# Performance work log

Measured on AMD Instinct MI355X. Metric: run time of the kernel, lower is better.

Reference implementation:

```python
import jax, jax.numpy as jnp
import numpy as np

N_LAYERS, B, H, D = 24, 16, 32, 64
E = H * D            # 2048
TS_H = 32            # token_shift_hidden_dim
N_BRANCH = 5         # key, receptance, decay, value, bonus
GN_EPS = 1e-3        # keras GroupNormalization default epsilon


def setup_inputs() -> dict:
    key = jax.random.key(0)
    ks = jax.random.split(key, 20)
    s = 0.02
    return {
        "inputs": jax.random.normal(ks[0], (B, E), jnp.float32),
        "state": jax.random.normal(ks[1], (N_LAYERS, 1, B, E), jnp.float32),
        "state_matrix": jax.random.normal(ks[2], (N_LAYERS, B, H, D, D), jnp.float32),
        # stacked branch params, order: key, receptance, decay, value, bonus
        "mus": jax.random.normal(ks[3], (N_BRANCH, E), jnp.float32) * s,
        "lambdas": jax.random.normal(ks[4], (N_BRANCH, E), jnp.float32) * s,
        "Aw": jax.random.normal(ks[5], (N_BRANCH, E, TS_H), jnp.float32) * s,
        "Ab": jnp.zeros((N_BRANCH, TS_H), jnp.float32),
        "Bw": jax.random.normal(ks[6], (N_BRANCH, TS_H, E), jnp.float32) * s,
        "Bb": jnp.zeros((N_BRANCH, E), jnp.float32),
        "MW": jax.random.normal(ks[7], (N_BRANCH, H, D, D), jnp.float32) * s,
        "Mb": jnp.zeros((N_BRANCH, H, D), jnp.float32),
        "gate_mu": jax.random.normal(ks[8], (E,), jnp.float32) * s,
        "gate_W": jax.random.normal(ks[9], (E, E), jnp.float32) * s,
        "gate_b": jnp.zeros((E,), jnp.float32),
        "gn_gamma": jnp.ones((E,), jnp.float32),
        "gn_beta": jnp.zeros((E,), jnp.float32),
        "out_W": jax.random.normal(ks[10], (E, E), jnp.float32) * s,
        "out_b": jnp.zeros((E,), jnp.float32),
        "layer_id": 12,
    }


def reference(inputs, state, state_matrix, mus, lambdas, Aw, Ab, Bw, Bb, MW, Mb,
              gate_mu, gate_W, gate_b, gn_gamma, gn_beta, out_W, out_b, layer_id):
    x = inputs                       # [B, E]
    last_x = state[layer_id, 0]      # [B, E]
    diff = x - last_x

    # ddlerp token shift for all 5 branches at once:
    # lora(x + diff*mu) = lambda + tanh(. @ A) @ B ; out = x + lora * diff
    lora_in = x[None] + diff[None] * mus[:, None]                      # [5, B, E]
    hdn = jnp.tanh(jnp.einsum('sbe,seh->sbh', lora_in, Aw) + Ab[:, None])
    lora = jnp.einsum('sbh,she->sbe', hdn, Bw) + Bb[:, None] + lambdas[:, None]
    ts = (lora * diff[None] + x[None]).reshape(N_BRANCH, B, H, D)      # [5, B, H, D]

    # per-head dense for each branch
    proj = jnp.einsum('sbhd,shde->sbhe', ts, MW) + Mb[:, None]         # [5, B, H, D]
    k, r, w_raw, v, u = proj[0], proj[1], proj[2], proj[3], proj[4]

    g = (x * gate_mu + last_x * (1.0 - gate_mu)) @ gate_W + gate_b     # [B, E]

    kv = k[..., :, None] * v[..., None, :]                             # [B, H, D, D]
    w = jnp.exp(-jnp.exp(w_raw))[..., None]                            # [B, H, D, 1]
    S = state_matrix[layer_id]                                         # [B, H, D, D]
    wkv = kv * u[..., None] + S
    new_S = w * S + kv
    rwkv = jnp.einsum('bhij,bhj->bhi', wkv, r)                         # [B, H, D]

    # group norm: num_heads groups over channel axis
    mean = rwkv.mean(-1, keepdims=True)
    var = rwkv.var(-1, keepdims=True)
    normed = ((rwkv - mean) / jnp.sqrt(var + GN_EPS)).reshape(B, E)
    normed = normed * gn_gamma + gn_beta

    time_mixed = (normed * jax.nn.silu(g)) @ out_W + out_b             # [B, E]

    new_state = state.at[layer_id, 0].set(inputs)
    new_state_matrix = state_matrix.at[layer_id].set(new_S)
    return time_mixed, new_state, new_state_matrix
```

## Files before the change

kernel.cpp:

```cpp
#include <hip/hip_runtime.h>
#include <math.h>

#define NL 24
#define BB 16
#define HH 32
#define DD 64
#define EE 2048
#define TSH 32
#define NB 5
#define BE (BB*EE)
#define STATE_N (NL*BB*EE)
#define SM_N (NL*BB*HH*DD*DD)
#define GN_EPS 1e-3f

__global__ __launch_bounds__(256) void k_head(
    const float4* __restrict__ state4, const float4* __restrict__ inputs4,
    float4* __restrict__ out_state4,
    float* __restrict__ out_tm, float* __restrict__ g,
    const float* __restrict__ out_b, const float* __restrict__ gate_b,
    const float* __restrict__ inputs, const float* __restrict__ state,
    const float* __restrict__ mus, const float* __restrict__ Aw,
    const float* __restrict__ Ab, const float* __restrict__ lambdas,
    const float* __restrict__ Bw, const float* __restrict__ Bb,
    const float* __restrict__ MW, const float* __restrict__ Mb,
    const float* __restrict__ gate_mu, float* __restrict__ proj,
    float* __restrict__ gx, const int* __restrict__ lid_p)
{
    int blk = blockIdx.x, tid = threadIdx.x;
    int lid = *lid_p;
    if (blk < 768) {
        int i = blk * 256 + tid;
        int lo = lid * (BE / 4);
        float4 v = (i >= lo && i < lo + BE / 4) ? inputs4[i - lo] : state4[i];
        out_state4[i] = v;
        return;
    }
    if (blk < 1024) {
        int idx = (blk - 768) * 256 + tid;
        if (idx < BE) out_tm[idx] = out_b[idx & (EE - 1)];
        else g[idx - BE] = gate_b[(idx - BE) & (EE - 1)];
        return;
    }
    int sb = blk - 1024;
    int s = sb / BB, b = sb % BB;
    __shared__ float xs[EE], dsh[EE], lis[EE], tsl[EE];
    __shared__ float red[TSH][9];
    __shared__ float hdnl[TSH];
    const float* x  = inputs + b * EE;
    const float* lx = state + lid * BE + b * EE;
    const float* mu = mus + s * EE;
    for (int e = tid; e < EE; e += 256) {
        float xv = x[e], lxv = lx[e];
        float d = xv - lxv;
        xs[e] = xv; dsh[e] = d;
        lis[e] = xv + d * mu[e];
        if (s == 0) {
            float gm = gate_mu[e];
            gx[b * EE + e] = xv * gm + lxv * (1.f - gm);
        }
    }
    __syncthreads();
    {
        int h = tid & 31, part = tid >> 5;
        const float* A = Aw + s * EE * TSH;
        float acc = 0.f;
        int e0 = part * 256;
        #pragma unroll 8
        for (int e = e0; e < e0 + 256; ++e) acc += lis[e] * A[e * TSH + h];
        red[h][part] = acc;
    }
    __syncthreads();
    if (tid < TSH) {
        float sum = Ab[s * TSH + tid];
        #pragma unroll
        for (int p = 0; p < 8; ++p) sum += red[tid][p];
        hdnl[tid] = tanhf(sum);
    }
    __syncthreads();
    for (int e = tid; e < EE; e += 256) {
        const float* Bp = Bw + s * TSH * EE + e;
        float acc = Bb[s * EE + e] + lambdas[s * EE + e];
        #pragma unroll
        for (int h2 = 0; h2 < TSH; ++h2) acc += hdnl[h2] * Bp[h2 * EE];
        tsl[e] = acc * dsh[e] + xs[e];
    }
    __syncthreads();
    for (int o = tid; o < EE; o += 256) {
        int h2 = o >> 6, e = o & 63;
        const float* M = MW + (s * HH + h2) * DD * DD;
        const float* t = tsl + h2 * DD;
        float acc = Mb[(s * HH + h2) * DD + e];
        #pragma unroll 8
        for (int d = 0; d < DD; ++d) acc += t[d] * M[d * DD + e];
        proj[(s * BB + b) * EE + o] = acc;
    }
}

template <bool SILU>
__device__ __forceinline__ void mm_block(
    int blk, const float* __restrict__ Arows, const float* __restrict__ Grows,
    const float* __restrict__ W, float* __restrict__ out)
{
    int tid = threadIdx.x;
    int et = blk & 7, kc = blk >> 3;
    int e = et * 256 + tid;
    int k0 = kc * 64;
    __shared__ float As[BB][64];
    for (int i = tid; i < BB * 64; i += 256) {
        int b = i >> 6, kk = i & 63;
        float av = Arows[b * EE + k0 + kk];
        if constexpr (SILU) {
            float gv = Grows[b * EE + k0 + kk];
            av *= gv / (1.f + expf(-gv));
        }
        As[b][kk] = av;
    }
    __syncthreads();
    float acc[BB];
    #pragma unroll
    for (int b = 0; b < BB; ++b) acc[b] = 0.f;
    #pragma unroll 8
    for (int kk = 0; kk < 64; ++kk) {
        float wv = W[(k0 + kk) * EE + e];
        #pragma unroll
        for (int b = 0; b < BB; ++b) acc[b] += As[b][kk] * wv;
    }
    #pragma unroll
    for (int b = 0; b < BB; ++b) atomicAdd(&out[b * EE + e], acc[b]);
}

__global__ __launch_bounds__(256) void k_mid(
    const float* __restrict__ gx, const float* __restrict__ gate_W,
    float* __restrict__ g,
    const float4* __restrict__ sm4, float4* __restrict__ out_sm4,
    const float* __restrict__ proj,
    const float* __restrict__ gn_gamma, const float* __restrict__ gn_beta,
    float* __restrict__ a_out, const int* __restrict__ lid_p)
{
    int blk = blockIdx.x, tid = threadIdx.x;
    if (blk < 256) { mm_block<false>(blk, gx, nullptr, gate_W, g); return; }
    int lid = *lid_p;
    int r = blk - 256;
    int b = r / HH, h = r % HH;
    int base4 = (lid * BB * HH + r) * (DD * DD / 4);
    int j = tid & 63, q = tid >> 6;
    const float* P = proj + (b * HH + h) * DD + j;
    float kv   = P[0 * BE];
    float rv   = P[1 * BE];
    float wraw = P[2 * BE];
    float vv   = P[3 * BE];
    float uv   = P[4 * BE];
    float wv = expf(-expf(wraw));
    float vr = vv * rv;
    #pragma unroll
    for (int o = 32; o; o >>= 1) vr += __shfl_xor(vr, o);
    __shared__ float rw[DD];
    const float* S = (const float*)(sm4 + base4);
    float* NS = (float*)(out_sm4 + base4);
    for (int ii = 0; ii < 16; ii += 4) {
        int i0 = q * 16 + ii;
        float sv[4], kk[4], ww[4], uu[4], pp[4];
        #pragma unroll
        for (int t = 0; t < 4; ++t) {
            sv[t] = S[(i0 + t) * DD + j];
            kk[t] = __shfl(kv, i0 + t);
            ww[t] = __shfl(wv, i0 + t);
            uu[t] = __shfl(uv, i0 + t);
        }
        #pragma unroll
        for (int t = 0; t < 4; ++t) {
            NS[(i0 + t) * DD + j] = ww[t] * sv[t] + kk[t] * vv;
            pp[t] = sv[t] * rv;
        }
        #pragma unroll
        for (int o = 32; o; o >>= 1) {
            #pragma unroll
            for (int t = 0; t < 4; ++t) pp[t] += __shfl_xor(pp[t], o);
        }
        if (j == 0) {
            #pragma unroll
            for (int t = 0; t < 4; ++t) rw[i0 + t] = kk[t] * uu[t] * vr + pp[t];
        }
    }
    __syncthreads();
    if (tid < DD) {
        float xv = rw[tid];
        float m = xv;
        #pragma unroll
        for (int o = 32; o; o >>= 1) m += __shfl_xor(m, o);
        m *= (1.f / 64.f);
        float d = xv - m;
        float var = d * d;
        #pragma unroll
        for (int o = 32; o; o >>= 1) var += __shfl_xor(var, o);
        var *= (1.f / 64.f);
        float normed = d * rsqrtf(var + GN_EPS);
        int e = h * DD + tid;
        a_out[b * EE + e] = normed * gn_gamma[e] + gn_beta[e];
    }
}

__global__ __launch_bounds__(256) void k_tail(
    const float* __restrict__ a, const float* __restrict__ g,
    const float* __restrict__ out_W, float* __restrict__ out_tm,
    const float4* __restrict__ sm4, float4* __restrict__ out_sm4,
    const int* __restrict__ lid_p)
{
    int blk = blockIdx.x, tid = threadIdx.x;
    if (blk < 256) { mm_block<true>(blk, a, g, out_W, out_tm); return; }
    int lid = *lid_p;
    int c = blk - 256;
    int l = c >> 9;
    int rr = c & 511;
    int ls = l + (l >= lid);
    const float4* src = sm4 + ((long)ls * 512 + rr) * 1024;
    float4* dst = out_sm4 + ((long)ls * 512 + rr) * 1024;
    #pragma unroll
    for (int p = 0; p < 4; ++p) dst[p * 256 + tid] = src[p * 256 + tid];
}

extern "C" void kernel_launch(void* const* d_in, const int* in_sizes, int n_in,
                              void* d_out, int out_size, void* d_ws, size_t ws_size,
                              hipStream_t stream) {
    const float* inputs   = (const float*)d_in[0];
    const float* state    = (const float*)d_in[1];
    const float* sm       = (const float*)d_in[2];
    const float* mus      = (const float*)d_in[3];
    const float* lambdas  = (const float*)d_in[4];
    const float* Aw       = (const float*)d_in[5];
    const float* Ab       = (const float*)d_in[6];
    const float* Bw       = (const float*)d_in[7];
    const float* Bb       = (const float*)d_in[8];
    const float* MW       = (const float*)d_in[9];
    const float* Mb       = (const float*)d_in[10];
    const float* gate_mu  = (const float*)d_in[11];
    const float* gate_W   = (const float*)d_in[12];
    const float* gate_b   = (const float*)d_in[13];
    const float* gn_gamma = (const float*)d_in[14];
    const float* gn_beta  = (const float*)d_in[15];
    const float* out_W    = (const float*)d_in[16];
    const float* out_b    = (const float*)d_in[17];
    const int*   lid      = (const int*)d_in[18];

    float* out_tm    = (float*)d_out;
    float* out_state = out_tm + BE;
    float* out_sm    = out_state + STATE_N;

    float* ws   = (float*)d_ws;
    float* proj = ws;
    float* gx   = proj + NB * BE;
    float* g    = gx + BE;
    float* a    = g + BE;

    k_head<<<1104, 256, 0, stream>>>((const float4*)state, (const float4*)inputs,
                                     (float4*)out_state, out_tm, g, out_b, gate_b,
                                     inputs, state, mus, Aw, Ab, lambdas, Bw, Bb,
                                     MW, Mb, gate_mu, proj, gx, lid);
    k_mid<<<768, 256, 0, stream>>>(gx, gate_W, g, (const float4*)sm, (float4*)out_sm,
                                   proj, gn_gamma, gn_beta, a, lid);
    k_tail<<<12032, 256, 0, stream>>>(a, g, out_W, out_tm,
                                      (const float4*)sm, (float4*)out_sm, lid);
}
```

Before: 470.5 us.

## Split head into three kernels and spread state-matrix copy across all launches

The monolithic head kernel, which ran 80 serial-heavy blocks, is split into three stages: hidden tanh, token-shift LoRA expansion and per-head projection. Each stage now uses many more parallel blocks. The bulk copy of the unchanged state-matrix layers is cut into chunks and attached to every one of the six launches, so the bandwidth-bound copy runs alongside the latency-bound compute stages instead of all at the end. The cost is more kernel launches and intermediate round-trips through workspace memory.

```diff
diff --git a/kernel.cpp b/kernel.cpp
--- a/kernel.cpp
+++ b/kernel.cpp
@@ -10,99 +10,148 @@
 #define NB 5
 #define BE (BB*EE)
 #define STATE_N (NL*BB*EE)
-#define SM_N (NL*BB*HH*DD*DD)
 #define GN_EPS 1e-3f
 
-__global__ __launch_bounds__(256) void k_head(
-    const float4* __restrict__ state4, const float4* __restrict__ inputs4,
-    float4* __restrict__ out_state4,
-    float* __restrict__ out_tm, float* __restrict__ g,
-    const float* __restrict__ out_b, const float* __restrict__ gate_b,
+#define NCH 11776
+#define C1 2400
+#define C2 2200
+#define C3 2400
+#define C4 2200
+#define C5 1776
+#define C6 800
+
+__device__ __forceinline__ void sm_chunk(int c, int lid, const float4* __restrict__ sm4,
+                                         float4* __restrict__ out4, int tid) {
+    int l = c >> 9, rr = c & 511;
+    int ls = l + (l >= lid);
+    const float4* src = sm4 + (long)(ls * 512 + rr) * 1024;
+    float4*       dst = out4 + (long)(ls * 512 + rr) * 1024;
+    #pragma unroll
+    for (int p = 0; p < 4; ++p) dst[p * 256 + tid] = src[p * 256 + tid];
+}
+
+__global__ __launch_bounds__(256) void k1_hdn(
     const float* __restrict__ inputs, const float* __restrict__ state,
     const float* __restrict__ mus, const float* __restrict__ Aw,
-    const float* __restrict__ Ab, const float* __restrict__ lambdas,
-    const float* __restrict__ Bw, const float* __restrict__ Bb,
-    const float* __restrict__ MW, const float* __restrict__ Mb,
-    const float* __restrict__ gate_mu, float* __restrict__ proj,
-    float* __restrict__ gx, const int* __restrict__ lid_p)
-{
-    int blk = blockIdx.x, tid = threadIdx.x;
-    int lid = *lid_p;
-    if (blk < 768) {
-        int i = blk * 256 + tid;
+    const float* __restrict__ Ab, float* __restrict__ hdn,
+    const float4* __restrict__ state4, const float4* __restrict__ inputs4,
+    float4* __restrict__ out_state4, float* __restrict__ out_tm,
+    float* __restrict__ g, const float* __restrict__ out_b,
+    const float* __restrict__ gate_b,
+    const float4* __restrict__ sm4, float4* __restrict__ out_sm4,
+    const int* __restrict__ lid_p)
+{
+    int blk = blockIdx.x, tid = threadIdx.x;
+    int lid = *lid_p;
+    if (blk >= 1104) {
+        sm_chunk(blk - 1104, lid, sm4, out_sm4, tid);
+        return;
+    }
+    if (blk >= 848) {
+        int idx = (blk - 848) * 256 + tid;
+        if (idx < BE) out_tm[idx] = out_b[idx & (EE - 1)];
+        else g[idx - BE] = gate_b[(idx - BE) & (EE - 1)];
+        return;
+    }
+    if (blk >= 80) {
+        int i = (blk - 80) * 256 + tid;
         int lo = lid * (BE / 4);
         float4 v = (i >= lo && i < lo + BE / 4) ? inputs4[i - lo] : state4[i];
         out_state4[i] = v;
         return;
     }
-    if (blk < 1024) {
-        int idx = (blk - 768) * 256 + tid;
-        if (idx < BE) out_tm[idx] = out_b[idx & (EE - 1)];
-        else g[idx - BE] = gate_b[(idx - BE) & (EE - 1)];
-        return;
-    }
-    int sb = blk - 1024;
-    int s = sb / BB, b = sb % BB;
-    __shared__ float xs[EE], dsh[EE], lis[EE], tsl[EE];
-    __shared__ float red[TSH][9];
-    __shared__ float hdnl[TSH];
+    int s = blk / BB, b = blk % BB;
+    __shared__ float li[EE];
     const float* x  = inputs + b * EE;
     const float* lx = state + lid * BE + b * EE;
     const float* mu = mus + s * EE;
     for (int e = tid; e < EE; e += 256) {
-        float xv = x[e], lxv = lx[e];
-        float d = xv - lxv;
-        xs[e] = xv; dsh[e] = d;
-        lis[e] = xv + d * mu[e];
-        if (s == 0) {
-            float gm = gate_mu[e];
-            gx[b * EE + e] = xv * gm + lxv * (1.f - gm);
-        }
-    }
-    __syncthreads();
-    {
-        int h = tid & 31, part = tid >> 5;
-        const float* A = Aw + s * EE * TSH;
-        float acc = 0.f;
-        int e0 = part * 256;
-        #pragma unroll 8
-        for (int e = e0; e < e0 + 256; ++e) acc += lis[e] * A[e * TSH + h];
-        red[h][part] = acc;
-    }
-    __syncthreads();
-    if (tid < TSH) {
+        float xv = x[e];
+        li[e] = xv + (xv - lx[e]) * mu[e];
+    }
+    __syncthreads();
+    int h = tid & 31, part = tid >> 5;
+    const float* A = Aw + s * EE * TSH;
+    float acc = 0.f;
+    int e0 = part * 256;
+    #pragma unroll 8
+    for (int e = e0; e < e0 + 256; ++e) acc += li[e] * A[e * TSH + h];
+    __shared__ float red[32][9];
+    red[h][part] = acc;
+    __syncthreads();
+    if (tid < 32) {
         float sum = Ab[s * TSH + tid];
         #pragma unroll
         for (int p = 0; p < 8; ++p) sum += red[tid][p];
-        hdnl[tid] = tanhf(sum);
-    }
-    __syncthreads();
-    for (int e = tid; e < EE; e += 256) {
-        const float* Bp = Bw + s * TSH * EE + e;
-        float acc = Bb[s * EE + e] + lambdas[s * EE + e];
-        #pragma unroll
-        for (int h2 = 0; h2 < TSH; ++h2) acc += hdnl[h2] * Bp[h2 * EE];
-        tsl[e] = acc * dsh[e] + xs[e];
-    }
-    __syncthreads();
-    for (int o = tid; o < EE; o += 256) {
-        int h2 = o >> 6, e = o & 63;
-        const float* M = MW + (s * HH + h2) * DD * DD;
-        const float* t = tsl + h2 * DD;
-        float acc = Mb[(s * HH + h2) * DD + e];
-        #pragma unroll 8
-        for (int d = 0; d < DD; ++d) acc += t[d] * M[d * DD + e];
-        proj[(s * BB + b) * EE + o] = acc;
-    }
+        hdn[(s * BB + b) * TSH + tid] = tanhf(sum);
+    }
+}
+
+__global__ __launch_bounds__(256) void k2_ts(
+    const float* __restrict__ inputs, const float* __restrict__ state,
+    const float* __restrict__ lambdas, const float* __restrict__ Bw,
+    const float* __restrict__ Bb, const float* __restrict__ hdn,
+    const float* __restrict__ gate_mu, float* __restrict__ ts,
+    float* __restrict__ gx,
+    const float4* __restrict__ sm4, float4* __restrict__ out_sm4,
+    const int* __restrict__ lid_p)
+{
+    int blk = blockIdx.x, tid = threadIdx.x;
+    int lid = *lid_p;
+    if (blk >= 640) {
+        sm_chunk(C1 + blk - 640, lid, sm4, out_sm4, tid);
+        return;
+    }
+    int idx = blk * 256 + tid;
+    int s = idx / BE, r = idx % BE;
+    int b = r / EE, e = r % EE;
+    const float* hp = hdn + (s * BB + b) * TSH;
+    const float* Bp = Bw + s * TSH * EE + e;
+    float acc = Bb[s * EE + e] + lambdas[s * EE + e];
+    #pragma unroll
+    for (int h = 0; h < TSH; ++h) acc += hp[h] * Bp[h * EE];
+    float xv = inputs[r];
+    float lxv = state[lid * BE + r];
+    ts[idx] = acc * (xv - lxv) + xv;
+    if (s == 0) {
+        float gm = gate_mu[e];
+        gx[r] = xv * gm + lxv * (1.f - gm);
+    }
+}
+
+__global__ __launch_bounds__(256) void k3_proj(
+    const float* __restrict__ ts, const float* __restrict__ MW,
+    const float* __restrict__ Mb, float* __restrict__ proj,
+    const float4* __restrict__ sm4, float4* __restrict__ out_sm4,
+    const int* __restrict__ lid_p)
+{
+    int bi = blockIdx.x, tid = threadIdx.x;
+    if (bi >= 640) {
+        int lid = *lid_p;
+        sm_chunk(C1 + C2 + bi - 640, lid, sm4, out_sm4, tid);
+        return;
+    }
+    int s = bi / (BB * 8);
+    int r = bi % (BB * 8);
+    int b = r / 8, hg = r % 8;
+    int q = tid >> 6, e = tid & 63;
+    int h = hg * 4 + q;
+    __shared__ float tl[4][DD];
+    tl[q][e] = ts[((s * BB + b) * HH + h) * DD + e];
+    __syncthreads();
+    const float* M = MW + (s * HH + h) * DD * DD;
+    float acc = Mb[(s * HH + h) * DD + e];
+    #pragma unroll 8
+    for (int d = 0; d < DD; ++d) acc += tl[q][d] * M[d * DD + e];
+    proj[((s * BB + b) * HH + h) * DD + e] = acc;
 }
 
 template <bool SILU>
 __device__ __forceinline__ void mm_block(
-    int blk, const float* __restrict__ Arows, const float* __restrict__ Grows,
-    const float* __restrict__ W, float* __restrict__ out)
-{
-    int tid = threadIdx.x;
-    int et = blk & 7, kc = blk >> 3;
+    int t, const float* __restrict__ Arows, const float* __restrict__ Grows,
+    const float* __restrict__ W, float* __restrict__ out, int tid)
+{
+    int et = t & 7, kc = t >> 3;
     int e = et * 256 + tid;
     int k0 = kc * 64;
     __shared__ float As[BB][64];
@@ -129,20 +178,32 @@
     for (int b = 0; b < BB; ++b) atomicAdd(&out[b * EE + e], acc[b]);
 }
 
-__global__ __launch_bounds__(256) void k_mid(
+__global__ __launch_bounds__(256) void k4_gate(
     const float* __restrict__ gx, const float* __restrict__ gate_W,
     float* __restrict__ g,
+    const float4* __restrict__ sm4, float4* __restrict__ out_sm4,
+    const int* __restrict__ lid_p)
+{
+    int blk = blockIdx.x, tid = threadIdx.x;
+    if (blk < 256) { mm_block<false>(blk, gx, nullptr, gate_W, g, tid); return; }
+    int lid = *lid_p;
+    sm_chunk(C1 + C2 + C3 + blk - 256, lid, sm4, out_sm4, tid);
+}
+
+__global__ __launch_bounds__(256) void k5_rwkv(
     const float4* __restrict__ sm4, float4* __restrict__ out_sm4,
     const float* __restrict__ proj,
     const float* __restrict__ gn_gamma, const float* __restrict__ gn_beta,
     float* __restrict__ a_out, const int* __restrict__ lid_p)
 {
     int blk = blockIdx.x, tid = threadIdx.x;
-    if (blk < 256) { mm_block<false>(blk, gx, nullptr, gate_W, g); return; }
-    int lid = *lid_p;
-    int r = blk - 256;
-    int b = r / HH, h = r % HH;
-    int base4 = (lid * BB * HH + r) * (DD * DD / 4);
+    int lid = *lid_p;
+    if (blk >= 512) {
+        sm_chunk(C1 + C2 + C3 + C4 + blk - 512, lid, sm4, out_sm4, tid);
+        return;
+    }
+    int b = blk / HH, h = blk % HH;
+    long base4 = (long)(lid * BB * HH + blk) * (DD * DD / 4);
     int j = tid & 63, q = tid >> 6;
     const float* P = proj + (b * HH + h) * DD + j;
     float kv   = P[0 * BE];
@@ -200,23 +261,16 @@
     }
 }
 
-__global__ __launch_bounds__(256) void k_tail(
+__global__ __launch_bounds__(256) void k6_out(
     const float* __restrict__ a, const float* __restrict__ g,
     const float* __restrict__ out_W, float* __restrict__ out_tm,
     const float4* __restrict__ sm4, float4* __restrict__ out_sm4,
     const int* __restrict__ lid_p)
 {
     int blk = blockIdx.x, tid = threadIdx.x;
-    if (blk < 256) { mm_block<true>(blk, a, g, out_W, out_tm); return; }
-    int lid = *lid_p;
-    int c = blk - 256;
-    int l = c >> 9;
-    int rr = c & 511;
-    int ls = l + (l >= lid);
-    const float4* src = sm4 + ((long)ls * 512 + rr) * 1024;
-    float4* dst = out_sm4 + ((long)ls * 512 + rr) * 1024;
-    #pragma unroll
-    for (int p = 0; p < 4; ++p) dst[p * 256 + tid] = src[p * 256 + tid];
+    if (blk < 256) { mm_block<true>(blk, a, g, out_W, out_tm, tid); return; }
+    int lid = *lid_p;
+    sm_chunk(C1 + C2 + C3 + C4 + C5 + blk - 256, lid, sm4, out_sm4, tid);
 }
 
 extern "C" void kernel_launch(void* const* d_in, const int* in_sizes, int n_in,
@@ -247,17 +301,24 @@
     float* out_sm    = out_state + STATE_N;
 
     float* ws   = (float*)d_ws;
-    float* proj = ws;
-    float* gx   = proj + NB * BE;
+    float* ts   = ws;
+    float* proj = ts + NB * BE;
+    float* hdn  = proj + NB * BE;
+    float* gx   = hdn + NB * BB * TSH;
     float* g    = gx + BE;
     float* a    = g + BE;
 
-    k_head<<<1104, 256, 0, stream>>>((const float4*)state, (const float4*)inputs,
-                                     (float4*)out_state, out_tm, g, out_b, gate_b,
-                                     inputs, state, mus, Aw, Ab, lambdas, Bw, Bb,
-                                     MW, Mb, gate_mu, proj, gx, lid);
-    k_mid<<<768, 256, 0, stream>>>(gx, gate_W, g, (const float4*)sm, (float4*)out_sm,
-                                   proj, gn_gamma, gn_beta, a, lid);
-    k_tail<<<12032, 256, 0, stream>>>(a, g, out_W, out_tm,
-                                      (const float4*)sm, (float4*)out_sm, lid);
-}
+    k1_hdn<<<1104 + C1, 256, 0, stream>>>(inputs, state, mus, Aw, Ab, hdn,
+        (const float4*)state, (const float4*)inputs, (float4*)out_state,
+        out_tm, g, out_b, gate_b, (const float4*)sm, (float4*)out_sm, lid);
+    k2_ts<<<640 + C2, 256, 0, stream>>>(inputs, state, lambdas, Bw, Bb, hdn,
+        gate_mu, ts, gx, (const float4*)sm, (float4*)out_sm, lid);
+    k3_proj<<<640 + C3, 256, 0, stream>>>(ts, MW, Mb, proj,
+        (const float4*)sm, (float4*)out_sm, lid);
+    k4_gate<<<256 + C4, 256, 0, stream>>>(gx, gate_W, g,
+        (const float4*)sm, (float4*)out_sm, lid);
+    k5_rwkv<<<512 + C5, 256, 0, stream>>>((const float4*)sm, (float4*)out_sm,
+        proj, gn_gamma, gn_beta, a, lid);
+    k6_out<<<256 + C6, 256, 0, stream>>>(a, g, out_W, out_tm,
+        (const float4*)sm, (float4*)out_sm, lid);
+}
```

Result: faster. 442.5 us (-5.9%).
